# Performance work log

Measured on AMD Instinct MI355X. Metric: run time of the kernel, lower is better.

## Reference

```python
import jax, jax.numpy as jnp
import numpy as np

N = 50000      # nodes
E = 800000     # edges
F = 128        # num_features
DIM = 128      # dim
NF = 4         # n_factor
ND = DIM // NF # n_dim = 32
NL = 3         # n_layer
NC = 10        # n_class
G = 256        # num graphs in batch


def setup_inputs() -> dict:
    key = jax.random.key(0)
    ks = jax.random.split(key, 20)
    w = lambda k, shape, fan: (jax.random.normal(k, shape, jnp.float32) / np.sqrt(fan)).astype(jnp.float32)
    inp = {}
    inp["x"] = jax.random.normal(ks[0], (N, F), jnp.float32)
    inp["edge_index"] = jax.random.randint(ks[1], (2, E), 0, N)
    inp["batch"] = jnp.sort(jax.random.randint(ks[2], (N,), 0, G))
    # attention branch: lin0 (F->DIM) and att linear (2*DIM -> 1) per factor
    inp["lin0_W"] = w(ks[3], (NF, F, DIM), F)
    inp["lin0_b"] = jnp.zeros((NF, DIM), jnp.float32)
    inp["att_W"] = w(ks[4], (NF, 2 * DIM), 2 * DIM)
    inp["att_b"] = jnp.zeros((NF,), jnp.float32)
    # encoder per-factor input linear (F -> ND)
    inp["enc_W"] = w(ks[5], (NF, F, ND), F)
    inp["enc_b"] = jnp.zeros((NF, ND), jnp.float32)
    # GraphConv per factor/layer: lin_rel (with bias) + lin_root (no bias)
    inp["conv_Wrel"] = w(ks[6], (NF, NL, ND, ND), ND)
    inp["conv_brel"] = jnp.zeros((NF, NL, ND), jnp.float32)
    inp["conv_Wroot"] = w(ks[7], (NF, NL, ND, ND), ND)
    # GRU per factor (input ND, hidden ND), torch layout: [3*H, in]
    inp["gru_Wih"] = w(ks[8], (NF, 3 * ND, ND), ND)
    inp["gru_Whh"] = w(ks[9], (NF, 3 * ND, ND), ND)
    inp["gru_bih"] = jnp.zeros((NF, 3 * ND), jnp.float32)
    inp["gru_bhh"] = jnp.zeros((NF, 3 * ND), jnp.float32)
    # head
    inp["fc1_W"] = w(ks[10], (DIM, DIM), DIM)
    inp["fc1_b"] = jnp.zeros((DIM,), jnp.float32)
    inp["fc2_W"] = w(ks[11], (DIM, NC), DIM)
    inp["fc2_b"] = jnp.zeros((NC,), jnp.float32)
    return inp


def _gru_step(m, h, Wih, Whh, bih, bhh):
    # torch GRUCell math; gates order [r, z, n]
    gi = m @ Wih.T + bih   # [N, 3H]
    gh = h @ Whh.T + bhh
    ir, iz, inn = jnp.split(gi, 3, axis=-1)
    hr, hz, hn = jnp.split(gh, 3, axis=-1)
    r = jax.nn.sigmoid(ir + hr)
    z = jax.nn.sigmoid(iz + hz)
    n = jnp.tanh(inn + r * hn)
    return (1.0 - z) * n + z * h


def reference(x, edge_index, batch, lin0_W, lin0_b, att_W, att_b, enc_W, enc_b,
              conv_Wrel, conv_brel, conv_Wroot, gru_Wih, gru_Whh, gru_bih, gru_bhh,
              fc1_W, fc1_b, fc2_W, fc2_b):
    src, dst = edge_index[0], edge_index[1]
    counts = jnp.maximum(jax.ops.segment_sum(jnp.ones((N,), jnp.float32), batch, num_segments=G), 1.0)
    outs, atts = [], []
    for f in range(NF):
        # edge attention: sigmoid(6 * Linear([lin0(x[src]) || lin0(x[dst])]))
        a = x @ lin0_W[f] + lin0_b[f]                     # [N, DIM]
        Wl, Wr = att_W[f, :DIM], att_W[f, DIM:]
        e = a[src] @ Wl + a[dst] @ Wr + att_b[f]          # [E]
        att_i = jax.nn.sigmoid(6.0 * e)
        atts.append(att_i)
        # disentangled encoder for this factor
        out = x @ enc_W[f] + enc_b[f]                     # [N, ND]
        h = out
        for l in range(NL):
            # GraphConv: lin_rel(scatter_add(x[src]*w -> dst)) + lin_root(x)
            msg = out[src] * att_i[:, None]               # [E, ND]
            agg = jax.ops.segment_sum(msg, dst, num_segments=N)
            m = jax.nn.relu(agg @ conv_Wrel[f, l] + conv_brel[f, l] + out @ conv_Wroot[f, l])
            h = _gru_step(m, h, gru_Wih[f], gru_Whh[f], gru_bih[f], gru_bhh[f])
            out = h
        pooled = jax.ops.segment_sum(out, batch, num_segments=G) / counts[:, None]  # [G, ND]
        outs.append(pooled)
    out_cat = jnp.concatenate(outs, axis=-1)              # [G, DIM]
    pred = jax.nn.relu(out_cat @ fc1_W + fc1_b) @ fc2_W + fc2_b  # [G, NC]
    return pred, jnp.stack(atts, 0), jnp.stack(outs, 0)
```

## Files before the change

### kernel.cpp

```cpp
#include <hip/hip_runtime.h>
#include <hip/hip_fp16.h>
#include <math.h>

#define N   50000
#define E   800000
#define F   128
#define DIM 128
#define NF  4
#define ND  32
#define NL  3
#define NC  10
#define G   256
#define NB  196

typedef __attribute__((ext_vector_type(8))) short  s16x8;
typedef __attribute__((ext_vector_type(4))) float  f32x4;

__device__ __forceinline__ float sigm(float v) { return 1.0f / (1.0f + __expf(-v)); }

__device__ __forceinline__ unsigned int f2bf(float x) {
    unsigned int u = __float_as_uint(x);
    return (u + 0x7FFFu + ((u >> 16) & 1u)) >> 16;
}

__device__ __forceinline__ void split8(const float* v, s16x8& hi, s16x8& lo) {
    #pragma unroll
    for (int i = 0; i < 8; ++i) {
        float x = v[i];
        unsigned int h = f2bf(x);
        float hf = __uint_as_float(h << 16);
        hi[i] = (short)h;
        lo[i] = (short)f2bf(x - hf);
    }
}

#define MFMA(a, b, c) c = __builtin_amdgcn_mfma_f32_16x16x32_bf16(a, b, c, 0, 0, 0)
#define MF3(xh, xl, wh, wl, c) do { MFMA(xh, wh, c); MFMA(xh, wl, c); MFMA(xl, wh, c); } while (0)

__global__ void prep_kernel(const float* __restrict__ lin0_W, const float* __restrict__ lin0_b,
                            const float* __restrict__ att_W, const float* __restrict__ att_b,
                            float* __restrict__ vl, float* __restrict__ vr, float* __restrict__ cc) {
    int t = blockIdx.x * blockDim.x + threadIdx.x;
    if (t < NF * F) {
        int f = t >> 7, k = t & 127;
        const float* W  = lin0_W + (size_t)f * F * DIM + (size_t)k * DIM;
        const float* wl = att_W + f * 2 * DIM;
        const float* wr = wl + DIM;
        float sl = 0.f, sr = 0.f;
        for (int j = 0; j < DIM; ++j) { sl += W[j] * wl[j]; sr += W[j] * wr[j]; }
        vl[t] = sl; vr[t] = sr;
    }
    if (t < NF) {
        const float* b  = lin0_b + t * DIM;
        const float* wl = att_W + t * 2 * DIM;
        const float* wr = wl + DIM;
        float s = att_b[t];
        for (int j = 0; j < DIM; ++j) s += b[j] * (wl[j] + wr[j]);
        cc[t] = s;
    }
}

__global__ void wfrag_kernel(const float* __restrict__ Wrel, const float* __restrict__ Wroot,
                             const float* __restrict__ Wih, const float* __restrict__ Whh,
                             const float* __restrict__ enc_W,
                             const float* __restrict__ vl, const float* __restrict__ vr,
                             unsigned short* __restrict__ convfrag,
                             unsigned short* __restrict__ grufrag,
                             unsigned short* __restrict__ encfrag,
                             unsigned short* __restrict__ attfrag) {
    int b = blockIdx.x;
    int l = threadIdx.x;
    int lr = l & 15, lg = l >> 4;
    if (b < 12) {
        const float* wrelg  = Wrel  + (size_t)b * 1024;
        const float* wrootg = Wroot + (size_t)b * 1024;
        #pragma unroll
        for (int H = 0; H < 2; ++H) {
            #pragma unroll
            for (int i = 0; i < 8; ++i) {
                float x = wrelg[(lg * 8 + i) * 32 + H * 16 + lr];
                unsigned int h = f2bf(x);
                convfrag[(((size_t)b * 8 + 0 + H) * 64 + l) * 8 + i] = (unsigned short)h;
                convfrag[(((size_t)b * 8 + 2 + H) * 64 + l) * 8 + i] =
                    (unsigned short)f2bf(x - __uint_as_float(h << 16));
                x = wrootg[(lg * 8 + i) * 32 + H * 16 + lr];
                h = f2bf(x);
                convfrag[(((size_t)b * 8 + 4 + H) * 64 + l) * 8 + i] = (unsigned short)h;
                convfrag[(((size_t)b * 8 + 6 + H) * 64 + l) * 8 + i] =
                    (unsigned short)f2bf(x - __uint_as_float(h << 16));
            }
        }
    } else if (b < 16) {
        int f = b - 12;
        const float* wihg = Wih + (size_t)f * 3072;
        const float* whhg = Whh + (size_t)f * 3072;
        #pragma unroll
        for (int m = 0; m < 6; ++m) {
            const float* base = (m < 3 ? wihg : whhg) + (size_t)((m % 3) * 32) * 32;
            #pragma unroll
            for (int H = 0; H < 2; ++H) {
                int col = H * 16 + lr;
                #pragma unroll
                for (int i = 0; i < 8; ++i) {
                    float x = base[(size_t)col * 32 + lg * 8 + i];
                    unsigned int h = f2bf(x);
                    grufrag[(((size_t)(f * 6 + m) * 4 + H) * 64 + l) * 8 + i] = (unsigned short)h;
                    grufrag[(((size_t)(f * 6 + m) * 4 + 2 + H) * 64 + l) * 8 + i] =
                        (unsigned short)f2bf(x - __uint_as_float(h << 16));
                }
            }
        }
    } else {
        int f = b - 16;
        const float* we = enc_W + (size_t)f * F * ND;
        #pragma unroll
        for (int c = 0; c < 4; ++c) {
            #pragma unroll
            for (int i = 0; i < 8; ++i) {
                int k = c * 32 + lg * 8 + i;
                #pragma unroll
                for (int H = 0; H < 2; ++H) {
                    float x = we[(size_t)k * 32 + H * 16 + lr];
                    unsigned int h = f2bf(x);
                    encfrag[((((size_t)(f * 4 + c) * 2 + H) * 2 + 0) * 64 + l) * 8 + i] =
                        (unsigned short)h;
                    encfrag[((((size_t)(f * 4 + c) * 2 + H) * 2 + 1) * 64 + l) * 8 + i] =
                        (unsigned short)f2bf(x - __uint_as_float(h << 16));
                }
                float av = (lr == 0) ? vl[f * F + k] : (lr == 1) ? vr[f * F + k] : 0.f;
                unsigned int ha = f2bf(av);
                attfrag[(((size_t)(f * 4 + c) * 2 + 0) * 64 + l) * 8 + i] = (unsigned short)ha;
                attfrag[(((size_t)(f * 4 + c) * 2 + 1) * 64 + l) * 8 + i] =
                    (unsigned short)f2bf(av - __uint_as_float(ha << 16));
            }
        }
    }
}

__global__ __launch_bounds__(256) void encode_kernel(
        const float* __restrict__ x,
        const unsigned short* __restrict__ encfrag,
        const unsigned short* __restrict__ attfrag,
        const float* __restrict__ enc_b,
        float* __restrict__ out, unsigned short* __restrict__ st16,
        float* __restrict__ alr) {
    int tid = threadIdx.x;
    int f  = __builtin_amdgcn_readfirstlane(tid >> 6);
    int l  = tid & 63;
    int lr = l & 15, lg = l >> 4;
    int node0 = blockIdx.x * 32;

    s16x8 beh[4][2], bel[4][2], bah[4], bal[4];
    #pragma unroll
    for (int c = 0; c < 4; ++c) {
        #pragma unroll
        for (int H = 0; H < 2; ++H) {
            beh[c][H] = *(const s16x8*)&encfrag[((((size_t)(f*4 + c)*2 + H)*2 + 0)*64 + l)*8];
            bel[c][H] = *(const s16x8*)&encfrag[((((size_t)(f*4 + c)*2 + H)*2 + 1)*64 + l)*8];
        }
        bah[c] = *(const s16x8*)&attfrag[(((size_t)(f*4 + c)*2 + 0)*64 + l)*8];
        bal[c] = *(const s16x8*)&attfrag[(((size_t)(f*4 + c)*2 + 1)*64 + l)*8];
    }
    float be0 = enc_b[f*32 + lr], be1 = enc_b[f*32 + 16 + lr];

    #pragma unroll
    for (int s = 0; s < 2; ++s) {
        int n0 = node0 + s * 16;
        int na = n0 + lr; int nac = na < N ? na : N - 1;
        const float* px = x + (size_t)nac * F + lg * 8;
        s16x8 xh[4], xl[4];
        #pragma unroll
        for (int c = 0; c < 4; ++c) {
            float v[8];
            float4 q0 = *(const float4*)(px + c * 32);
            float4 q1 = *(const float4*)(px + c * 32 + 4);
            v[0]=q0.x; v[1]=q0.y; v[2]=q0.z; v[3]=q0.w; v[4]=q1.x; v[5]=q1.y; v[6]=q1.z; v[7]=q1.w;
            split8(v, xh[c], xl[c]);
        }
        f32x4 o0 = {be0, be0, be0, be0};
        f32x4 o1 = {be1, be1, be1, be1};
        f32x4 ca = {0.f, 0.f, 0.f, 0.f};
        #pragma unroll
        for (int c = 0; c < 4; ++c) {
            MF3(xh[c], xl[c], beh[c][0], bel[c][0], o0);
            MF3(xh[c], xl[c], beh[c][1], bel[c][1], o1);
            MF3(xh[c], xl[c], bah[c],    bal[c],    ca);
        }
        #pragma unroll
        for (int j = 0; j < 4; ++j) {
            int n = n0 + lg * 4 + j;
            if (n < N) {
                out[(size_t)n * DIM + f * ND + lr]       = o0[j];
                out[(size_t)n * DIM + f * ND + 16 + lr]  = o1[j];
                st16[(size_t)n * DIM + f * ND + lr]      = (unsigned short)f2bf(o0[j]);
                st16[(size_t)n * DIM + f * ND + 16 + lr] = (unsigned short)f2bf(o1[j]);
                if (lr == 0)      alr[(size_t)n * 8 + f]     = ca[j];
                else if (lr == 1) alr[(size_t)n * 8 + 4 + f] = ca[j];
            }
        }
    }
}

__global__ void hist_kernel(const int* __restrict__ ei, int* __restrict__ deg) {
    int e = blockIdx.x * 256 + threadIdx.x;
    if (e < E) atomicAdd(&deg[ei[E + e]], 1);
}

__global__ void scan1_kernel(const int* __restrict__ deg, int* __restrict__ rowp,
                             int* __restrict__ bsum) {
    __shared__ int sh[256];
    int i = blockIdx.x * 256 + threadIdx.x;
    int v = (i < N) ? deg[i] : 0;
    sh[threadIdx.x] = v;
    __syncthreads();
    for (int off = 1; off < 256; off <<= 1) {
        int t = 0;
        if ((int)threadIdx.x >= off) t = sh[threadIdx.x - off];
        __syncthreads();
        sh[threadIdx.x] += t;
        __syncthreads();
    }
    if (i < N) rowp[i] = sh[threadIdx.x] - v;
    if (threadIdx.x == 255) bsum[blockIdx.x] = sh[255];
}

__global__ void scan2_kernel(int* __restrict__ bsum) {
    __shared__ int sh[256];
    int v = ((int)threadIdx.x < NB) ? bsum[threadIdx.x] : 0;
    sh[threadIdx.x] = v;
    __syncthreads();
    for (int off = 1; off < 256; off <<= 1) {
        int t = 0;
        if ((int)threadIdx.x >= off) t = sh[threadIdx.x - off];
        __syncthreads();
        sh[threadIdx.x] += t;
        __syncthreads();
    }
    if ((int)threadIdx.x < NB) bsum[threadIdx.x] = sh[threadIdx.x] - v;
}

__global__ void scan3_kernel(int* __restrict__ rowp, const int* __restrict__ bsum) {
    int i = blockIdx.x * 256 + threadIdx.x;
    if (i < N) rowp[i] += bsum[i >> 8];
}

__global__ void fill_kernel(const int* __restrict__ ei, const float* __restrict__ alr,
                            const float* __restrict__ cc,
                            const int* __restrict__ rowp, int* __restrict__ cnt,
                            uint4* __restrict__ erec, float* __restrict__ atts) {
    int e = blockIdx.x * 256 + threadIdx.x;
    if (e >= E) return;
    int s = ei[e];
    int d = ei[E + e];
    float4 al = *(const float4*)(alr + (size_t)s * 8);
    float4 ar = *(const float4*)(alr + (size_t)d * 8 + 4);
    float a0 = sigm(6.f * (al.x + ar.x + cc[0]));
    float a1 = sigm(6.f * (al.y + ar.y + cc[1]));
    float a2 = sigm(6.f * (al.z + ar.z + cc[2]));
    float a3 = sigm(6.f * (al.w + ar.w + cc[3]));
    atts[e]                 = a0;
    atts[(size_t)E + e]     = a1;
    atts[2 * (size_t)E + e] = a2;
    atts[3 * (size_t)E + e] = a3;
    unsigned int p01 = (unsigned int)__half_as_ushort(__float2half(a0))
                     | ((unsigned int)__half_as_ushort(__float2half(a1)) << 16);
    unsigned int p23 = (unsigned int)__half_as_ushort(__float2half(a2))
                     | ((unsigned int)__half_as_ushort(__float2half(a3)) << 16);
    int slot = rowp[d] + atomicAdd(&cnt[d], 1);
    erec[slot] = make_uint4((unsigned int)s, p01, p23, 0u);
}

__global__ __launch_bounds__(256) void gather_kernel(
        const uint4* __restrict__ erec,
        const int* __restrict__ rowp, const int* __restrict__ deg,
        const unsigned short* __restrict__ st16,
        unsigned int* __restrict__ agghi, unsigned int* __restrict__ agglo) {
    int gw = (blockIdx.x << 2) | ((int)threadIdx.x >> 6);
    int n = __builtin_amdgcn_readfirstlane(gw);
    int lane = threadIdx.x & 63;
    int f = lane >> 4;
    int beg = rowp[n];
    int cnt = deg[n];
    const uint4* rp4 = erec + beg;
    const int fhi = f >> 1;
    const int ash = (f & 1) * 16;
    const unsigned short* ob = st16 + lane * 2;
    float ax = 0.f, ay = 0.f;
    int i = 0;
    #define REXT(r) __half2float(__ushort_as_half((unsigned short)(((fhi ? (r).z : (r).y)) >> ash)))
    for (; i + 8 <= cnt; i += 8) {
        uint4 r0 = rp4[i],     r1 = rp4[i + 1], r2 = rp4[i + 2], r3 = rp4[i + 3];
        uint4 r4 = rp4[i + 4], r5 = rp4[i + 5], r6 = rp4[i + 6], r7 = rp4[i + 7];
        float a0 = REXT(r0), a1 = REXT(r1), a2 = REXT(r2), a3 = REXT(r3);
        float a4 = REXT(r4), a5 = REXT(r5), a6 = REXT(r6), a7 = REXT(r7);
        unsigned int u0 = *(const unsigned int*)(ob + (size_t)r0.x * DIM);
        unsigned int u1 = *(const unsigned int*)(ob + (size_t)r1.x * DIM);
        unsigned int u2 = *(const unsigned int*)(ob + (size_t)r2.x * DIM);
        unsigned int u3 = *(const unsigned int*)(ob + (size_t)r3.x * DIM);
        unsigned int u4 = *(const unsigned int*)(ob + (size_t)r4.x * DIM);
        unsigned int u5 = *(const unsigned int*)(ob + (size_t)r5.x * DIM);
        unsigned int u6 = *(const unsigned int*)(ob + (size_t)r6.x * DIM);
        unsigned int u7 = *(const unsigned int*)(ob + (size_t)r7.x * DIM);
        ax += a0 * __uint_as_float(u0 << 16) + a1 * __uint_as_float(u1 << 16)
            + a2 * __uint_as_float(u2 << 16) + a3 * __uint_as_float(u3 << 16)
            + a4 * __uint_as_float(u4 << 16) + a5 * __uint_as_float(u5 << 16)
            + a6 * __uint_as_float(u6 << 16) + a7 * __uint_as_float(u7 << 16);
        ay += a0 * __uint_as_float(u0 & 0xFFFF0000u) + a1 * __uint_as_float(u1 & 0xFFFF0000u)
            + a2 * __uint_as_float(u2 & 0xFFFF0000u) + a3 * __uint_as_float(u3 & 0xFFFF0000u)
            + a4 * __uint_as_float(u4 & 0xFFFF0000u) + a5 * __uint_as_float(u5 & 0xFFFF0000u)
            + a6 * __uint_as_float(u6 & 0xFFFF0000u) + a7 * __uint_as_float(u7 & 0xFFFF0000u);
    }
    for (; i + 4 <= cnt; i += 4) {
        uint4 r0 = rp4[i], r1 = rp4[i + 1], r2 = rp4[i + 2], r3 = rp4[i + 3];
        float a0 = REXT(r0), a1 = REXT(r1), a2 = REXT(r2), a3 = REXT(r3);
        unsigned int u0 = *(const unsigned int*)(ob + (size_t)r0.x * DIM);
        unsigned int u1 = *(const unsigned int*)(ob + (size_t)r1.x * DIM);
        unsigned int u2 = *(const unsigned int*)(ob + (size_t)r2.x * DIM);
        unsigned int u3 = *(const unsigned int*)(ob + (size_t)r3.x * DIM);
        ax += a0 * __uint_as_float(u0 << 16) + a1 * __uint_as_float(u1 << 16)
            + a2 * __uint_as_float(u2 << 16) + a3 * __uint_as_float(u3 << 16);
        ay += a0 * __uint_as_float(u0 & 0xFFFF0000u) + a1 * __uint_as_float(u1 & 0xFFFF0000u)
            + a2 * __uint_as_float(u2 & 0xFFFF0000u) + a3 * __uint_as_float(u3 & 0xFFFF0000u);
    }
    for (; i < cnt; ++i) {
        uint4 r = rp4[i];
        float a = REXT(r);
        unsigned int u = *(const unsigned int*)(ob + (size_t)r.x * DIM);
        ax += a * __uint_as_float(u << 16);
        ay += a * __uint_as_float(u & 0xFFFF0000u);
    }
    #undef REXT
    unsigned int hx = f2bf(ax), hy = f2bf(ay);
    float fx = __uint_as_float(hx << 16), fy = __uint_as_float(hy << 16);
    agghi[(size_t)n * 64 + lane] = hx | (hy << 16);
    agglo[(size_t)n * 64 + lane] = f2bf(ax - fx) | (f2bf(ay - fy) << 16);
}

__global__ __launch_bounds__(256) void update_kernel(
        const unsigned int* __restrict__ agghi, const unsigned int* __restrict__ agglo,
        float* __restrict__ out, unsigned short* __restrict__ st16,
        const unsigned short* __restrict__ convfrag, const unsigned short* __restrict__ grufrag,
        const float* __restrict__ brel,
        const float* __restrict__ bih, const float* __restrict__ bhh, int lay) {
    __shared__ __align__(16) unsigned short mls[NF][2][2][16 * 40];
    int tid = threadIdx.x;
    int f   = __builtin_amdgcn_readfirstlane(tid >> 6);
    int l   = tid & 63;
    int lr  = l & 15;
    int lg  = l >> 4;
    int node0 = blockIdx.x * 32;

    const unsigned short* cf = convfrag + (size_t)(f * NL + lay) * 8 * 64 * 8;
    s16x8 wrelh[2], wrell[2], wrooth[2], wrootl[2];
    #pragma unroll
    for (int H = 0; H < 2; ++H) {
        wrelh[H]  = *(const s16x8*)&cf[((0 + H) * 64 + l) * 8];
        wrell[H]  = *(const s16x8*)&cf[((2 + H) * 64 + l) * 8];
        wrooth[H] = *(const s16x8*)&cf[((4 + H) * 64 + l) * 8];
        wrootl[H] = *(const s16x8*)&cf[((6 + H) * 64 + l) * 8];
    }
    const unsigned short* gf = grufrag + (size_t)f * 6 * 4 * 64 * 8;
    s16x8 wirh[2], wirl[2], wizh[2], wizl[2], winh[2], winl[2];
    s16x8 whrh[2], whrl[2], whzh[2], whzl[2], whnh[2], whnl[2];
    #pragma unroll
    for (int H = 0; H < 2; ++H) {
        wirh[H] = *(const s16x8*)&gf[((0 * 4 + H) * 64 + l) * 8];
        wirl[H] = *(const s16x8*)&gf[((0 * 4 + 2 + H) * 64 + l) * 8];
        wizh[H] = *(const s16x8*)&gf[((1 * 4 + H) * 64 + l) * 8];
        wizl[H] = *(const s16x8*)&gf[((1 * 4 + 2 + H) * 64 + l) * 8];
        winh[H] = *(const s16x8*)&gf[((2 * 4 + H) * 64 + l) * 8];
        winl[H] = *(const s16x8*)&gf[((2 * 4 + 2 + H) * 64 + l) * 8];
        whrh[H] = *(const s16x8*)&gf[((3 * 4 + H) * 64 + l) * 8];
        whrl[H] = *(const s16x8*)&gf[((3 * 4 + 2 + H) * 64 + l) * 8];
        whzh[H] = *(const s16x8*)&gf[((4 * 4 + H) * 64 + l) * 8];
        whzl[H] = *(const s16x8*)&gf[((4 * 4 + 2 + H) * 64 + l) * 8];
        whnh[H] = *(const s16x8*)&gf[((5 * 4 + H) * 64 + l) * 8];
        whnl[H] = *(const s16x8*)&gf[((5 * 4 + 2 + H) * 64 + l) * 8];
    }

    float br_[2], bir_[2], biz_[2], bin_[2], bhn_[2];
    #pragma unroll
    for (int H = 0; H < 2; ++H) {
        int c = H * 16 + lr;
        br_[H]  = brel[(f * NL + lay) * 32 + c];
        bir_[H] = bih[f * 96 + c]      + bhh[f * 96 + c];
        biz_[H] = bih[f * 96 + 32 + c] + bhh[f * 96 + 32 + c];
        bin_[H] = bih[f * 96 + 64 + c];
        bhn_[H] = bhh[f * 96 + 64 + c];
    }

    const unsigned short* ahp = (const unsigned short*)agghi;
    const unsigned short* alp = (const unsigned short*)agglo;

    #pragma unroll
    for (int s = 0; s < 2; ++s) {
        int n0 = node0 + s * 16;
        unsigned short* mHi = &mls[f][s][0][0];
        unsigned short* mLo = &mls[f][s][1][0];
        int na  = n0 + lr;
        int nac = na < N ? na : N - 1;
        s16x8 aggH = *(const s16x8*)&ahp[(size_t)nac * DIM + f * ND + lg * 8];
        s16x8 aggL = *(const s16x8*)&alp[(size_t)nac * DIM + f * ND + lg * 8];
        const float* ph = out + (size_t)nac * DIM + f * ND + lg * 8;
        float vh[8];
        { float4 q0 = *(const float4*)ph, q1 = *(const float4*)(ph + 4);
          vh[0]=q0.x; vh[1]=q0.y; vh[2]=q0.z; vh[3]=q0.w; vh[4]=q1.x; vh[5]=q1.y; vh[6]=q1.z; vh[7]=q1.w; }
        s16x8 hH, hL;
        split8(vh, hH, hL);
        float hj0[4], hj1[4];
        #pragma unroll
        for (int j = 0; j < 4; ++j) {
            int nn_ = n0 + lg * 4 + j;
            int nnc = nn_ < N ? nn_ : N - 1;
            hj0[j] = out[(size_t)nnc * DIM + f * ND + lr];
            hj1[j] = out[(size_t)nnc * DIM + f * ND + 16 + lr];
        }

        f32x4 c0 = {br_[0], br_[0], br_[0], br_[0]};
        f32x4 c1 = {br_[1], br_[1], br_[1], br_[1]};
        MF3(aggH, aggL, wrelh[0],  wrell[0],  c0);
        MF3(hH,   hL,   wrooth[0], wrootl[0], c0);
        MF3(aggH, aggL, wrelh[1],  wrell[1],  c1);
        MF3(hH,   hL,   wrooth[1], wrootl[1], c1);

        #pragma unroll
        for (int j = 0; j < 4; ++j) {
            int row = lg * 4 + j;
            float v0 = fmaxf(c0[j], 0.f);
            float v1 = fmaxf(c1[j], 0.f);
            unsigned int h0 = f2bf(v0);
            unsigned int h1 = f2bf(v1);
            mHi[row * 40 + lr]      = (unsigned short)h0;
            mHi[row * 40 + 16 + lr] = (unsigned short)h1;
            mLo[row * 40 + lr]      = (unsigned short)f2bf(v0 - __uint_as_float(h0 << 16));
            mLo[row * 40 + 16 + lr] = (unsigned short)f2bf(v1 - __uint_as_float(h1 << 16));
        }
        __asm__ volatile("s_waitcnt lgkmcnt(0)" ::: "memory");
        __builtin_amdgcn_sched_barrier(0x37);
        s16x8 mH = *(const s16x8*)&mHi[lr * 40 + lg * 8];
        s16x8 mL = *(const s16x8*)&mLo[lr * 40 + lg * 8];

        f32x4 gr0 = {bir_[0], bir_[0], bir_[0], bir_[0]};
        f32x4 gr1 = {bir_[1], bir_[1], bir_[1], bir_[1]};
        f32x4 gz0 = {biz_[0], biz_[0], biz_[0], biz_[0]};
        f32x4 gz1 = {biz_[1], biz_[1], biz_[1], biz_[1]};
        f32x4 gn0 = {bin_[0], bin_[0], bin_[0], bin_[0]};
        f32x4 gn1 = {bin_[1], bin_[1], bin_[1], bin_[1]};
        f32x4 gh0 = {bhn_[0], bhn_[0], bhn_[0], bhn_[0]};
        f32x4 gh1 = {bhn_[1], bhn_[1], bhn_[1], bhn_[1]};
        MF3(mH, mL, wirh[0], wirl[0], gr0);  MF3(hH, hL, whrh[0], whrl[0], gr0);
        MF3(mH, mL, wirh[1], wirl[1], gr1);  MF3(hH, hL, whrh[1], whrl[1], gr1);
        MF3(mH, mL, wizh[0], wizl[0], gz0);  MF3(hH, hL, whzh[0], whzl[0], gz0);
        MF3(mH, mL, wizh[1], wizl[1], gz1);  MF3(hH, hL, whzh[1], whzl[1], gz1);
        MF3(mH, mL, winh[0], winl[0], gn0);
        MF3(mH, mL, winh[1], winl[1], gn1);
        MF3(hH, hL, whnh[0], whnl[0], gh0);
        MF3(hH, hL, whnh[1], whnl[1], gh1);

        #pragma unroll
        for (int j = 0; j < 4; ++j) {
            int n = n0 + lg * 4 + j;
            float r0 = sigm(gr0[j]);
            float z0 = sigm(gz0[j]);
            float t0 = 2.f * sigm(2.f * (gn0[j] + r0 * gh0[j])) - 1.f;
            float res0 = (1.f - z0) * t0 + z0 * hj0[j];
            float r1 = sigm(gr1[j]);
            float z1 = sigm(gz1[j]);
            float t1 = 2.f * sigm(2.f * (gn1[j] + r1 * gh1[j])) - 1.f;
            float res1 = (1.f - z1) * t1 + z1 * hj1[j];
            if (n < N) {
                out[(size_t)n * DIM + f * ND + lr]       = res0;
                out[(size_t)n * DIM + f * ND + 16 + lr]  = res1;
                st16[(size_t)n * DIM + f * ND + lr]      = (unsigned short)f2bf(res0);
                st16[(size_t)n * DIM + f * ND + 16 + lr] = (unsigned short)f2bf(res1);
            }
        }
    }
}

__global__ void goff_kernel(const int* __restrict__ batch, int* __restrict__ goff) {
    int g = threadIdx.x;
    int lo = 0, hi = N;
    while (lo < hi) {
        int mid = (lo + hi) >> 1;
        if (batch[mid] < g) lo = mid + 1; else hi = mid;
    }
    goff[g] = lo;
    if (g == 0) goff[G] = N;
}

__global__ void pool_kernel(const float* __restrict__ st, const int* __restrict__ goff,
                            float* __restrict__ pooled, float* __restrict__ outsout) {
    __shared__ float acc2[128];
    int g = blockIdx.x;
    int c = threadIdx.x & 127;
    int half = threadIdx.x >> 7;
    int beg = goff[g], cnt = goff[g + 1] - beg;
    float acc = 0.f;
    for (int i = half; i < cnt; i += 2) acc += st[(size_t)(beg + i) * DIM + c];
    if (half == 1) acc2[c] = acc;
    __syncthreads();
    if (half == 0) {
        float tot = acc + acc2[c];
        float val = tot / fmaxf((float)cnt, 1.0f);
        pooled[g * DIM + c] = val;
        int f = c >> 5, d = c & 31;
        outsout[((size_t)f * G + g) * ND + d] = val;
    }
}

__global__ void mlp_kernel(const float* __restrict__ pooled,
                           const float* __restrict__ fc1_W, const float* __restrict__ fc1_b,
                           const float* __restrict__ fc2_W, const float* __restrict__ fc2_b,
                           float* __restrict__ pred) {
    __shared__ float row[DIM], hid[DIM];
    int g = blockIdx.x, c = threadIdx.x;
    row[c] = pooled[(size_t)g * DIM + c];
    __syncthreads();
    float acc = fc1_b[c];
    #pragma unroll 8
    for (int k = 0; k < DIM; ++k) acc += row[k] * fc1_W[k * DIM + c];
    hid[c] = fmaxf(acc, 0.f);
    __syncthreads();
    if (c < NC) {
        float p = fc2_b[c];
        for (int k = 0; k < DIM; ++k) p += hid[k] * fc2_W[k * NC + c];
        pred[(size_t)g * NC + c] = p;
    }
}

extern "C" void kernel_launch(void* const* d_in, const int* in_sizes, int n_in,
                              void* d_out, int out_size, void* d_ws, size_t ws_size,
                              hipStream_t stream) {
    const float* x         = (const float*)d_in[0];
    const int*   ei        = (const int*)  d_in[1];
    const int*   batch     = (const int*)  d_in[2];
    const float* lin0_W    = (const float*)d_in[3];
    const float* lin0_b    = (const float*)d_in[4];
    const float* att_W     = (const float*)d_in[5];
    const float* att_b     = (const float*)d_in[6];
    const float* enc_W     = (const float*)d_in[7];
    const float* enc_b     = (const float*)d_in[8];
    const float* conv_Wrel = (const float*)d_in[9];
    const float* conv_brel = (const float*)d_in[10];
    const float* conv_Wroot= (const float*)d_in[11];
    const float* gru_Wih   = (const float*)d_in[12];
    const float* gru_Whh   = (const float*)d_in[13];
    const float* gru_bih   = (const float*)d_in[14];
    const float* gru_bhh   = (const float*)d_in[15];
    const float* fc1_W     = (const float*)d_in[16];
    const float* fc1_b     = (const float*)d_in[17];
    const float* fc2_W     = (const float*)d_in[18];
    const float* fc2_b     = (const float*)d_in[19];

    float* outp    = (float*)d_out;
    float* pred    = outp;
    float* atts    = outp + G * NC;
    float* outsout = atts + (size_t)NF * E;

    float* fp     = (float*)d_ws;
    float* st     = fp;                   fp += (size_t)N * DIM;
    unsigned int* agghi = (unsigned int*)fp;     fp += (size_t)N * 64;
    unsigned int* agglo = (unsigned int*)fp;     fp += (size_t)N * 64;
    unsigned short* st16 = (unsigned short*)fp;  fp += (size_t)N * DIM / 2;
    float* alr    = fp;                   fp += (size_t)N * 8;
    float* vl     = fp;                   fp += NF * F;
    float* vr     = fp;                   fp += NF * F;
    float* cc     = fp;                   fp += 4;
    float* pooled = fp;                   fp += G * DIM;
    unsigned short* convfrag = (unsigned short*)fp;  fp += 12 * 8 * 64 * 8 / 2;
    unsigned short* grufrag  = (unsigned short*)fp;  fp += 4 * 24 * 64 * 8 / 2;
    unsigned short* encfrag  = (unsigned short*)fp;  fp += 4 * 16 * 64 * 8 / 2;
    unsigned short* attfrag  = (unsigned short*)fp;  fp += 4 * 8 * 64 * 8 / 2;
    uint4* erec  = (uint4*)fp;            fp += (size_t)NF * E;
    int* ip    = (int*)fp;
    int* deg   = ip;                      ip += N;
    int* cnt   = ip;                      ip += N;
    int* rowp  = ip;                      ip += N;
    int* bsum  = ip;                      ip += 256;
    int* goff  = ip;                      ip += G + 1;

    hipMemsetAsync(deg, 0, (size_t)(2 * N) * sizeof(int), stream);

    prep_kernel<<<2, 256, 0, stream>>>(lin0_W, lin0_b, att_W, att_b, vl, vr, cc);
    wfrag_kernel<<<20, 64, 0, stream>>>(conv_Wrel, conv_Wroot, gru_Wih, gru_Whh,
                                        enc_W, vl, vr,
                                        convfrag, grufrag, encfrag, attfrag);
    goff_kernel<<<1, 256, 0, stream>>>(batch, goff);
    encode_kernel<<<(N + 31) / 32, 256, 0, stream>>>(x, encfrag, attfrag, enc_b,
                                                     st, st16, alr);

    hist_kernel<<<(E + 255) / 256, 256, 0, stream>>>(ei, deg);
    scan1_kernel<<<NB, 256, 0, stream>>>(deg, rowp, bsum);
    scan2_kernel<<<1, 256, 0, stream>>>(bsum);
    scan3_kernel<<<NB, 256, 0, stream>>>(rowp, bsum);
    fill_kernel<<<(E + 255) / 256, 256, 0, stream>>>(ei, alr, cc, rowp, cnt, erec, atts);

    for (int l = 0; l < NL; ++l) {
        gather_kernel<<<N / 4, 256, 0, stream>>>(erec, rowp, deg, st16, agghi, agglo);
        update_kernel<<<(N + 31) / 32, 256, 0, stream>>>(agghi, agglo, st, st16,
                                                         convfrag, grufrag, conv_brel,
                                                         gru_bih, gru_bhh, l);
    }

    pool_kernel<<<G, 256, 0, stream>>>(st, goff, pooled, outsout);
    mlp_kernel<<<G, DIM, 0, stream>>>(pooled, fc1_W, fc1_b, fc2_W, fc2_b, pred);
}
```

Measured before the change: 474.9 us.

## Merge setup kernels, fold scan3 into consumers, fuse pool+mlp, widen gather lanes

Merges prep, wfrag and goff into one setup kernel and fuses pool with the MLP head, cutting several small launches. The scan3 pass is removed by adding the block offset from bsum wherever rowp is read. The gather kernel now handles two nodes per wavefront, each lane loading 4 bf16 features with a uint2 load instead of 2. Fewer launches and wider loads reduce launch overhead and memory instructions, at the cost of one extra bsum load per node and a serial dot product inside the setup kernel.

```diff
diff --git a/kernel.cpp b/kernel.cpp
--- a/kernel.cpp
+++ b/kernel.cpp
@@ -37,39 +37,20 @@
 #define MFMA(a, b, c) c = __builtin_amdgcn_mfma_f32_16x16x32_bf16(a, b, c, 0, 0, 0)
 #define MF3(xh, xl, wh, wl, c) do { MFMA(xh, wh, c); MFMA(xh, wl, c); MFMA(xl, wh, c); } while (0)
 
-__global__ void prep_kernel(const float* __restrict__ lin0_W, const float* __restrict__ lin0_b,
-                            const float* __restrict__ att_W, const float* __restrict__ att_b,
-                            float* __restrict__ vl, float* __restrict__ vr, float* __restrict__ cc) {
-    int t = blockIdx.x * blockDim.x + threadIdx.x;
-    if (t < NF * F) {
-        int f = t >> 7, k = t & 127;
-        const float* W  = lin0_W + (size_t)f * F * DIM + (size_t)k * DIM;
-        const float* wl = att_W + f * 2 * DIM;
-        const float* wr = wl + DIM;
-        float sl = 0.f, sr = 0.f;
-        for (int j = 0; j < DIM; ++j) { sl += W[j] * wl[j]; sr += W[j] * wr[j]; }
-        vl[t] = sl; vr[t] = sr;
-    }
-    if (t < NF) {
-        const float* b  = lin0_b + t * DIM;
-        const float* wl = att_W + t * 2 * DIM;
-        const float* wr = wl + DIM;
-        float s = att_b[t];
-        for (int j = 0; j < DIM; ++j) s += b[j] * (wl[j] + wr[j]);
-        cc[t] = s;
-    }
-}
-
-__global__ void wfrag_kernel(const float* __restrict__ Wrel, const float* __restrict__ Wroot,
+__global__ void setup_kernel(const float* __restrict__ lin0_W, const float* __restrict__ lin0_b,
+                             const float* __restrict__ att_W, const float* __restrict__ att_b,
+                             const float* __restrict__ Wrel, const float* __restrict__ Wroot,
                              const float* __restrict__ Wih, const float* __restrict__ Whh,
-                             const float* __restrict__ enc_W,
-                             const float* __restrict__ vl, const float* __restrict__ vr,
+                             const float* __restrict__ enc_W, const int* __restrict__ batch,
                              unsigned short* __restrict__ convfrag,
                              unsigned short* __restrict__ grufrag,
                              unsigned short* __restrict__ encfrag,
-                             unsigned short* __restrict__ attfrag) {
+                             unsigned short* __restrict__ attfrag,
+                             float* __restrict__ cc, int* __restrict__ goff) {
     int b = blockIdx.x;
-    int l = threadIdx.x;
+    int tid = threadIdx.x;
+    if (b < 20 && tid >= 64) return;
+    int l = tid & 63;
     int lr = l & 15, lg = l >> 4;
     if (b < 12) {
         const float* wrelg  = Wrel  + (size_t)b * 1024;
@@ -110,7 +91,7 @@
                 }
             }
         }
-    } else {
+    } else if (b < 20) {
         int f = b - 16;
         const float* we = enc_W + (size_t)f * F * ND;
         #pragma unroll
@@ -127,13 +108,36 @@
                     encfrag[((((size_t)(f * 4 + c) * 2 + H) * 2 + 1) * 64 + l) * 8 + i] =
                         (unsigned short)f2bf(x - __uint_as_float(h << 16));
                 }
-                float av = (lr == 0) ? vl[f * F + k] : (lr == 1) ? vr[f * F + k] : 0.f;
+                float av = 0.f;
+                if (lr < 2) {
+                    const float* W  = lin0_W + (size_t)f * F * DIM + (size_t)k * DIM;
+                    const float* wv = att_W + f * 2 * DIM + lr * DIM;
+                    for (int j = 0; j < DIM; ++j) av += W[j] * wv[j];
+                }
                 unsigned int ha = f2bf(av);
                 attfrag[(((size_t)(f * 4 + c) * 2 + 0) * 64 + l) * 8 + i] = (unsigned short)ha;
                 attfrag[(((size_t)(f * 4 + c) * 2 + 1) * 64 + l) * 8 + i] =
                     (unsigned short)f2bf(av - __uint_as_float(ha << 16));
             }
         }
+    } else if (b == 20) {
+        if (tid < NF) {
+            const float* bb = lin0_b + tid * DIM;
+            const float* wl = att_W + tid * 2 * DIM;
+            const float* wr = wl + DIM;
+            float s = att_b[tid];
+            for (int j = 0; j < DIM; ++j) s += bb[j] * (wl[j] + wr[j]);
+            cc[tid] = s;
+        }
+    } else {
+        int g = tid;
+        int lo = 0, hi = N;
+        while (lo < hi) {
+            int mid = (lo + hi) >> 1;
+            if (batch[mid] < g) lo = mid + 1; else hi = mid;
+        }
+        goff[g] = lo;
+        if (g == 0) goff[G] = N;
     }
 }
 
@@ -239,14 +243,10 @@
     if ((int)threadIdx.x < NB) bsum[threadIdx.x] = sh[threadIdx.x] - v;
 }
 
-__global__ void scan3_kernel(int* __restrict__ rowp, const int* __restrict__ bsum) {
-    int i = blockIdx.x * 256 + threadIdx.x;
-    if (i < N) rowp[i] += bsum[i >> 8];
-}
-
 __global__ void fill_kernel(const int* __restrict__ ei, const float* __restrict__ alr,
                             const float* __restrict__ cc,
-                            const int* __restrict__ rowp, int* __restrict__ cnt,
+                            const int* __restrict__ rowp, const int* __restrict__ bsum,
+                            int* __restrict__ cnt,
                             uint4* __restrict__ erec, float* __restrict__ atts) {
     int e = blockIdx.x * 256 + threadIdx.x;
     if (e >= E) return;
@@ -266,74 +266,70 @@
                      | ((unsigned int)__half_as_ushort(__float2half(a1)) << 16);
     unsigned int p23 = (unsigned int)__half_as_ushort(__float2half(a2))
                      | ((unsigned int)__half_as_ushort(__float2half(a3)) << 16);
-    int slot = rowp[d] + atomicAdd(&cnt[d], 1);
+    int slot = rowp[d] + bsum[d >> 8] + atomicAdd(&cnt[d], 1);
     erec[slot] = make_uint4((unsigned int)s, p01, p23, 0u);
 }
 
 __global__ __launch_bounds__(256) void gather_kernel(
         const uint4* __restrict__ erec,
-        const int* __restrict__ rowp, const int* __restrict__ deg,
+        const int* __restrict__ rowp, const int* __restrict__ bsum,
+        const int* __restrict__ deg,
         const unsigned short* __restrict__ st16,
         unsigned int* __restrict__ agghi, unsigned int* __restrict__ agglo) {
-    int gw = (blockIdx.x << 2) | ((int)threadIdx.x >> 6);
-    int n = __builtin_amdgcn_readfirstlane(gw);
-    int lane = threadIdx.x & 63;
-    int f = lane >> 4;
-    int beg = rowp[n];
+    int tid  = threadIdx.x;
+    int lane = tid & 63;
+    int half = lane >> 5;
+    int l2   = lane & 31;
+    int n = blockIdx.x * 8 + ((tid >> 6) << 1) + half;
+    int beg = rowp[n] + bsum[n >> 8];
     int cnt = deg[n];
     const uint4* rp4 = erec + beg;
+    int f = l2 >> 3;
     const int fhi = f >> 1;
     const int ash = (f & 1) * 16;
-    const unsigned short* ob = st16 + lane * 2;
-    float ax = 0.f, ay = 0.f;
+    const unsigned short* ob = st16 + 4 * l2;
+    float s0 = 0.f, s1 = 0.f, s2 = 0.f, s3 = 0.f;
     int i = 0;
     #define REXT(r) __half2float(__ushort_as_half((unsigned short)(((fhi ? (r).z : (r).y)) >> ash)))
+    #define ROW(r)  (*(const uint2*)(ob + (size_t)(r).x * DIM))
+    #define ACC(a, u) do { \
+        s0 += (a) * __uint_as_float((u).x << 16); \
+        s1 += (a) * __uint_as_float((u).x & 0xFFFF0000u); \
+        s2 += (a) * __uint_as_float((u).y << 16); \
+        s3 += (a) * __uint_as_float((u).y & 0xFFFF0000u); } while (0)
     for (; i + 8 <= cnt; i += 8) {
         uint4 r0 = rp4[i],     r1 = rp4[i + 1], r2 = rp4[i + 2], r3 = rp4[i + 3];
         uint4 r4 = rp4[i + 4], r5 = rp4[i + 5], r6 = rp4[i + 6], r7 = rp4[i + 7];
+        uint2 u0 = ROW(r0), u1 = ROW(r1), u2 = ROW(r2), u3 = ROW(r3);
+        uint2 u4 = ROW(r4), u5 = ROW(r5), u6 = ROW(r6), u7 = ROW(r7);
         float a0 = REXT(r0), a1 = REXT(r1), a2 = REXT(r2), a3 = REXT(r3);
         float a4 = REXT(r4), a5 = REXT(r5), a6 = REXT(r6), a7 = REXT(r7);
-        unsigned int u0 = *(const unsigned int*)(ob + (size_t)r0.x * DIM);
-        unsigned int u1 = *(const unsigned int*)(ob + (size_t)r1.x * DIM);
-        unsigned int u2 = *(const unsigned int*)(ob + (size_t)r2.x * DIM);
-        unsigned int u3 = *(const unsigned int*)(ob + (size_t)r3.x * DIM);
-        unsigned int u4 = *(const unsigned int*)(ob + (size_t)r4.x * DIM);
-        unsigned int u5 = *(const unsigned int*)(ob + (size_t)r5.x * DIM);
-        unsigned int u6 = *(const unsigned int*)(ob + (size_t)r6.x * DIM);
-        unsigned int u7 = *(const unsigned int*)(ob + (size_t)r7.x * DIM);
-        ax += a0 * __uint_as_float(u0 << 16) + a1 * __uint_as_float(u1 << 16)
-            + a2 * __uint_as_float(u2 << 16) + a3 * __uint_as_float(u3 << 16)
-            + a4 * __uint_as_float(u4 << 16) + a5 * __uint_as_float(u5 << 16)
-            + a6 * __uint_as_float(u6 << 16) + a7 * __uint_as_float(u7 << 16);
-        ay += a0 * __uint_as_float(u0 & 0xFFFF0000u) + a1 * __uint_as_float(u1 & 0xFFFF0000u)
-            + a2 * __uint_as_float(u2 & 0xFFFF0000u) + a3 * __uint_as_float(u3 & 0xFFFF0000u)
-            + a4 * __uint_as_float(u4 & 0xFFFF0000u) + a5 * __uint_as_float(u5 & 0xFFFF0000u)
-            + a6 * __uint_as_float(u6 & 0xFFFF0000u) + a7 * __uint_as_float(u7 & 0xFFFF0000u);
+        ACC(a0, u0); ACC(a1, u1); ACC(a2, u2); ACC(a3, u3);
+        ACC(a4, u4); ACC(a5, u5); ACC(a6, u6); ACC(a7, u7);
     }
     for (; i + 4 <= cnt; i += 4) {
         uint4 r0 = rp4[i], r1 = rp4[i + 1], r2 = rp4[i + 2], r3 = rp4[i + 3];
+        uint2 u0 = ROW(r0), u1 = ROW(r1), u2 = ROW(r2), u3 = ROW(r3);
         float a0 = REXT(r0), a1 = REXT(r1), a2 = REXT(r2), a3 = REXT(r3);
-        unsigned int u0 = *(const unsigned int*)(ob + (size_t)r0.x * DIM);
-        unsigned int u1 = *(const unsigned int*)(ob + (size_t)r1.x * DIM);
-        unsigned int u2 = *(const unsigned int*)(ob + (size_t)r2.x * DIM);
-        unsigned int u3 = *(const unsigned int*)(ob + (size_t)r3.x * DIM);
-        ax += a0 * __uint_as_float(u0 << 16) + a1 * __uint_as_float(u1 << 16)
-            + a2 * __uint_as_float(u2 << 16) + a3 * __uint_as_float(u3 << 16);
-        ay += a0 * __uint_as_float(u0 & 0xFFFF0000u) + a1 * __uint_as_float(u1 & 0xFFFF0000u)
-            + a2 * __uint_as_float(u2 & 0xFFFF0000u) + a3 * __uint_as_float(u3 & 0xFFFF0000u);
+        ACC(a0, u0); ACC(a1, u1); ACC(a2, u2); ACC(a3, u3);
     }
     for (; i < cnt; ++i) {
         uint4 r = rp4[i];
+        uint2 u = ROW(r);
         float a = REXT(r);
-        unsigned int u = *(const unsigned int*)(ob + (size_t)r.x * DIM);
-        ax += a * __uint_as_float(u << 16);
-        ay += a * __uint_as_float(u & 0xFFFF0000u);
+        ACC(a, u);
     }
     #undef REXT
-    unsigned int hx = f2bf(ax), hy = f2bf(ay);
-    float fx = __uint_as_float(hx << 16), fy = __uint_as_float(hy << 16);
-    agghi[(size_t)n * 64 + lane] = hx | (hy << 16);
-    agglo[(size_t)n * 64 + lane] = f2bf(ax - fx) | (f2bf(ay - fy) << 16);
+    #undef ROW
+    #undef ACC
+    unsigned int h0 = f2bf(s0), h1 = f2bf(s1), h2 = f2bf(s2), h3 = f2bf(s3);
+    uint2 hi, lo;
+    hi.x = h0 | (h1 << 16);
+    hi.y = h2 | (h3 << 16);
+    lo.x = f2bf(s0 - __uint_as_float(h0 << 16)) | (f2bf(s1 - __uint_as_float(h1 << 16)) << 16);
+    lo.y = f2bf(s2 - __uint_as_float(h2 << 16)) | (f2bf(s3 - __uint_as_float(h3 << 16)) << 16);
+    *(uint2*)(agghi + (size_t)n * 64 + 2 * l2) = hi;
+    *(uint2*)(agglo + (size_t)n * 64 + 2 * l2) = lo;
 }
 
 __global__ __launch_bounds__(256) void update_kernel(
@@ -478,20 +474,13 @@
     }
 }
 
-__global__ void goff_kernel(const int* __restrict__ batch, int* __restrict__ goff) {
-    int g = threadIdx.x;
-    int lo = 0, hi = N;
-    while (lo < hi) {
-        int mid = (lo + hi) >> 1;
-        if (batch[mid] < g) lo = mid + 1; else hi = mid;
-    }
-    goff[g] = lo;
-    if (g == 0) goff[G] = N;
-}
-
-__global__ void pool_kernel(const float* __restrict__ st, const int* __restrict__ goff,
-                            float* __restrict__ pooled, float* __restrict__ outsout) {
-    __shared__ float acc2[128];
+__global__ void poolmlp_kernel(const float* __restrict__ st, const int* __restrict__ goff,
+                               const float* __restrict__ fc1_W, const float* __restrict__ fc1_b,
+                               const float* __restrict__ fc2_W, const float* __restrict__ fc2_b,
+                               float* __restrict__ pred, float* __restrict__ outsout) {
+    __shared__ float acc2[DIM];
+    __shared__ float row[DIM];
+    __shared__ float hid[DIM];
     int g = blockIdx.x;
     int c = threadIdx.x & 127;
     int half = threadIdx.x >> 7;
@@ -501,31 +490,23 @@
     if (half == 1) acc2[c] = acc;
     __syncthreads();
     if (half == 0) {
-        float tot = acc + acc2[c];
-        float val = tot / fmaxf((float)cnt, 1.0f);
-        pooled[g * DIM + c] = val;
+        float val = (acc + acc2[c]) / fmaxf((float)cnt, 1.0f);
+        row[c] = val;
         int f = c >> 5, d = c & 31;
         outsout[((size_t)f * G + g) * ND + d] = val;
     }
-}
-
-__global__ void mlp_kernel(const float* __restrict__ pooled,
-                           const float* __restrict__ fc1_W, const float* __restrict__ fc1_b,
-                           const float* __restrict__ fc2_W, const float* __restrict__ fc2_b,
-                           float* __restrict__ pred) {
-    __shared__ float row[DIM], hid[DIM];
-    int g = blockIdx.x, c = threadIdx.x;
-    row[c] = pooled[(size_t)g * DIM + c];
     __syncthreads();
-    float acc = fc1_b[c];
-    #pragma unroll 8
-    for (int k = 0; k < DIM; ++k) acc += row[k] * fc1_W[k * DIM + c];
-    hid[c] = fmaxf(acc, 0.f);
+    if (half == 0) {
+        float a = fc1_b[c];
+        #pragma unroll 8
+        for (int k = 0; k < DIM; ++k) a += row[k] * fc1_W[k * DIM + c];
+        hid[c] = fmaxf(a, 0.f);
+    }
     __syncthreads();
-    if (c < NC) {
-        float p = fc2_b[c];
-        for (int k = 0; k < DIM; ++k) p += hid[k] * fc2_W[k * NC + c];
-        pred[(size_t)g * NC + c] = p;
+    if (threadIdx.x < NC) {
+        float p = fc2_b[threadIdx.x];
+        for (int k = 0; k < DIM; ++k) p += hid[k] * fc2_W[k * NC + threadIdx.x];
+        pred[(size_t)g * NC + threadIdx.x] = p;
     }
 }
 
@@ -564,10 +545,7 @@
     unsigned int* agglo = (unsigned int*)fp;     fp += (size_t)N * 64;
     unsigned short* st16 = (unsigned short*)fp;  fp += (size_t)N * DIM / 2;
     float* alr    = fp;                   fp += (size_t)N * 8;
-    float* vl     = fp;                   fp += NF * F;
-    float* vr     = fp;                   fp += NF * F;
     float* cc     = fp;                   fp += 4;
-    float* pooled = fp;                   fp += G * DIM;
     unsigned short* convfrag = (unsigned short*)fp;  fp += 12 * 8 * 64 * 8 / 2;
     unsigned short* grufrag  = (unsigned short*)fp;  fp += 4 * 24 * 64 * 8 / 2;
     unsigned short* encfrag  = (unsigned short*)fp;  fp += 4 * 16 * 64 * 8 / 2;
@@ -582,27 +560,27 @@
 
     hipMemsetAsync(deg, 0, (size_t)(2 * N) * sizeof(int), stream);
 
-    prep_kernel<<<2, 256, 0, stream>>>(lin0_W, lin0_b, att_W, att_b, vl, vr, cc);
-    wfrag_kernel<<<20, 64, 0, stream>>>(conv_Wrel, conv_Wroot, gru_Wih, gru_Whh,
-                                        enc_W, vl, vr,
-                                        convfrag, grufrag, encfrag, attfrag);
-    goff_kernel<<<1, 256, 0, stream>>>(batch, goff);
+    setup_kernel<<<22, 256, 0, stream>>>(lin0_W, lin0_b, att_W, att_b,
+                                         conv_Wrel, conv_Wroot, gru_Wih, gru_Whh,
+                                         enc_W, batch,
+                                         convfrag, grufrag, encfrag, attfrag, cc, goff);
     encode_kernel<<<(N + 31) / 32, 256, 0, stream>>>(x, encfrag, attfrag, enc_b,
                                                      st, st16, alr);
 
     hist_kernel<<<(E + 255) / 256, 256, 0, stream>>>(ei, deg);
     scan1_kernel<<<NB, 256, 0, stream>>>(deg, rowp, bsum);
     scan2_kernel<<<1, 256, 0, stream>>>(bsum);
-    scan3_kernel<<<NB, 256, 0, stream>>>(rowp, bsum);
-    fill_kernel<<<(E + 255) / 256, 256, 0, stream>>>(ei, alr, cc, rowp, cnt, erec, atts);
+    fill_kernel<<<(E + 255) / 256, 256, 0, stream>>>(ei, alr, cc, rowp, bsum, cnt,
+                                                     erec, atts);
 
     for (int l = 0; l < NL; ++l) {
-        gather_kernel<<<N / 4, 256, 0, stream>>>(erec, rowp, deg, st16, agghi, agglo);
+        gather_kernel<<<N / 8, 256, 0, stream>>>(erec, rowp, bsum, deg, st16,
+                                                 agghi, agglo);
         update_kernel<<<(N + 31) / 32, 256, 0, stream>>>(agghi, agglo, st, st16,
                                                          convfrag, grufrag, conv_brel,
                                                          gru_bih, gru_bhh, l);
     }
 
-    pool_kernel<<<G, 256, 0, stream>>>(st, goff, pooled, outsout);
-    mlp_kernel<<<G, DIM, 0, stream>>>(pooled, fc1_W, fc1_b, fc2_W, fc2_b, pred);
-}
+    poolmlp_kernel<<<G, 256, 0, stream>>>(st, goff, fc1_W, fc1_b, fc2_W, fc2_b,
+                                          pred, outsout);
+}
```

Result: slower. 522.4 us (+10.0%).
